# Kernel tuning notes

Measured on AMD Instinct MI355X. Metric: run time of the kernel, lower is better.

The kernel has to match this reference:

```python
import jax, jax.numpy as jnp
import numpy as np

N = 50000
E = 800000
IN_CH = 128
HID = 32
HEADS = 8
OUT_CH = 64
NEG_SLOPE = 0.2


def _gat_layer(x, W, att_src, att_dst, bias, src, dst, H, C, concat):
    """One GATConv layer (add aggregation, self-loops appended).
    x: [n, Fin], W: [Fin, H*C], att_*: [H, C], bias: [H*C] or [C].
    src/dst: [E] int edge endpoints (no self loops; they are appended here).
    """
    n = x.shape[0]
    xs = (x @ W).reshape(n, H, C)                 # projected features [n,H,C]
    a_src = (xs * att_src).sum(-1)                # [n,H]
    a_dst = (xs * att_dst).sum(-1)                # [n,H]
    loop = jnp.arange(n, dtype=src.dtype)
    s = jnp.concatenate([src, loop])              # [E+n]
    d = jnp.concatenate([dst, loop])
    alpha = a_src[s] + a_dst[d]                   # per-edge score [E+n,H]
    alpha = jax.nn.leaky_relu(alpha, NEG_SLOPE)
    # segment softmax over destination node (every node has a self loop,
    # so no empty segments)
    amax = jax.ops.segment_max(alpha, d, num_segments=n)
    ex = jnp.exp(alpha - amax[d])
    denom = jax.ops.segment_sum(ex, d, num_segments=n)
    alpha = ex / denom[d]                         # normalized attention [E+n,H]
    # weighted scatter-add aggregation
    out = jax.ops.segment_sum(alpha[:, :, None] * xs[s], d, num_segments=n)
    out = out.reshape(n, H * C) if concat else out.mean(axis=1)
    return out + bias


def setup_inputs() -> dict:
    key = jax.random.key(0)
    ks = jax.random.split(key, 12)
    def glorot(k, shape):
        fan = shape[0] + shape[-1]
        return jax.random.uniform(k, shape, jnp.float32,
                                  -jnp.sqrt(6.0 / fan), jnp.sqrt(6.0 / fan))
    x = jax.random.normal(ks[0], (N, IN_CH), jnp.float32)
    edge_index = jax.random.randint(ks[1], (2, E), 0, N, dtype=jnp.int64)
    W1 = glorot(ks[2], (IN_CH, HEADS * HID))
    att_src1 = glorot(ks[3], (HEADS, HID))
    att_dst1 = glorot(ks[4], (HEADS, HID))
    bias1 = jnp.zeros((HEADS * HID,), jnp.float32)
    W2 = glorot(ks[5], (HEADS * HID, 1 * OUT_CH))
    att_src2 = glorot(ks[6], (1, OUT_CH))
    att_dst2 = glorot(ks[7], (1, OUT_CH))
    bias2 = jnp.zeros((OUT_CH,), jnp.float32)
    return {"x": x, "edge_index": edge_index,
            "W1": W1, "att_src1": att_src1, "att_dst1": att_dst1, "bias1": bias1,
            "W2": W2, "att_src2": att_src2, "att_dst2": att_dst2, "bias2": bias2}


def reference(x, edge_index, W1, att_src1, att_dst1, bias1,
              W2, att_src2, att_dst2, bias2):
    src, dst = edge_index[0], edge_index[1]
    h = _gat_layer(x, W1, att_src1, att_dst1, bias1, src, dst,
                   HEADS, HID, concat=True)      # [N, HEADS*HID]
    h = jax.nn.elu(h)
    out = _gat_layer(h, W2, att_src2, att_dst2, bias2, src, dst,
                     1, OUT_CH, concat=False)    # [N, OUT_CH]
    return out
```

## Files before the change

### kernel.cpp

```cpp
#include <hip/hip_runtime.h>

#define NN 50000
#define NE 800000
#define IN_CH 128
#define HID 32
#define HEADS 8
#define HC 256
#define OUT_CH 64
#define NEG_SLOPE 0.2f
#define SCAN_BLOCKS 196

typedef _Float16 half4 __attribute__((ext_vector_type(4)));
typedef _Float16 half8 __attribute__((ext_vector_type(8)));
typedef float    f32x4 __attribute__((ext_vector_type(4)));


__global__ void hist_kernel(const int* __restrict__ dst, int* __restrict__ deg) {
    int e = blockIdx.x * blockDim.x + threadIdx.x;
    if (e < NE) atomicAdd(&deg[dst[e]], 1);
}

__global__ __launch_bounds__(256)
void scan_phase1(const int* __restrict__ deg, int* __restrict__ excl,
                 int* __restrict__ bsum) {
    __shared__ int sm[256];
    const int t = blockIdx.x * 256 + threadIdx.x;
    const int v = (t < NN) ? deg[t] : 0;
    sm[threadIdx.x] = v;
    __syncthreads();
    for (int off = 1; off < 256; off <<= 1) {
        int u = (threadIdx.x >= off) ? sm[threadIdx.x - off] : 0;
        __syncthreads();
        sm[threadIdx.x] += u;
        __syncthreads();
    }
    if (t < NN) excl[t] = sm[threadIdx.x] - v;
    if (threadIdx.x == 255) bsum[blockIdx.x] = sm[255];
}

__global__ __launch_bounds__(256)
void scan_phase2(const int* __restrict__ bsum, int* __restrict__ boff,
                 int* __restrict__ offsets) {
    __shared__ int sm[256];
    const int t = threadIdx.x;
    const int v = (t < SCAN_BLOCKS) ? bsum[t] : 0;
    sm[t] = v;
    __syncthreads();
    for (int off = 1; off < 256; off <<= 1) {
        int u = (t >= off) ? sm[t - off] : 0;
        __syncthreads();
        sm[t] += u;
        __syncthreads();
    }
    if (t < SCAN_BLOCKS) boff[t] = sm[t] - v;
    if (t == 255) offsets[NN] = sm[255];
}

__global__ __launch_bounds__(256)
void scan_phase3(const int* __restrict__ excl, const int* __restrict__ boff,
                 int* __restrict__ offsets, int* __restrict__ cursor) {
    const int t = blockIdx.x * 256 + threadIdx.x;
    if (t < NN) {
        int v = excl[t] + boff[blockIdx.x];
        offsets[t] = v;
        cursor[t]  = v;
    }
}

__global__ void scatter_kernel(const int* __restrict__ src,
                               const int* __restrict__ dst,
                               int* __restrict__ cursor, int* __restrict__ ssrc) {
    int e = blockIdx.x * blockDim.x + threadIdx.x;
    if (e < NE) {
        int d = dst[e];
        int pos = atomicAdd(&cursor[d], 1);
        ssrc[pos] = src[e];
    }
}


__global__ void cast_f32_f16(const float* __restrict__ in, _Float16* __restrict__ out,
                             int n8) {
    int i = blockIdx.x * blockDim.x + threadIdx.x;
    if (i >= n8) return;
    float4 a = ((const float4*)in)[i * 2];
    float4 b = ((const float4*)in)[i * 2 + 1];
    half8 h;
    h[0] = (_Float16)a.x; h[1] = (_Float16)a.y; h[2] = (_Float16)a.z; h[3] = (_Float16)a.w;
    h[4] = (_Float16)b.x; h[5] = (_Float16)b.y; h[6] = (_Float16)b.z; h[7] = (_Float16)b.w;
    ((half8*)out)[i] = h;
}

__global__ void transpose_cast(const float* __restrict__ W, _Float16* __restrict__ Wt,
                               int K, int N) {
    int i = blockIdx.x * blockDim.x + threadIdx.x;
    if (i >= K * N) return;
    int k = i / N, n = i - k * N;
    Wt[(size_t)n * K + k] = (_Float16)W[i];
}

__global__ __launch_bounds__(256)
void gemm_mfma_h(const _Float16* __restrict__ A, const _Float16* __restrict__ Bt,
                 _Float16* __restrict__ C, int M, int N, int K) {
    __shared__ _Float16 Asl[64][136];
    __shared__ _Float16 Btl[64][136];
    const int tid  = threadIdx.x;
    const int wave = tid >> 6, lane = tid & 63;
    const int lr = lane & 15, lk = lane >> 4;
    const int bm = blockIdx.x * 64, bn = blockIdx.y * 64;
    const int sr = tid >> 2;
    const int ss = (tid & 3) * 32;

    f32x4 acc[4];
#pragma unroll
    for (int i = 0; i < 4; ++i) acc[i] = (f32x4){0.f, 0.f, 0.f, 0.f};

    for (int k0 = 0; k0 < K; k0 += 128) {
        {
            const int ar = bm + sr;
            half8 v0 = {}, v1 = {}, v2 = {}, v3 = {};
            if (ar < M) {
                const half8* ga = (const half8*)(A + (size_t)ar * K + k0 + ss);
                v0 = ga[0]; v1 = ga[1]; v2 = ga[2]; v3 = ga[3];
            }
            *(half8*)&Asl[sr][ss + 0]  = v0;
            *(half8*)&Asl[sr][ss + 8]  = v1;
            *(half8*)&Asl[sr][ss + 16] = v2;
            *(half8*)&Asl[sr][ss + 24] = v3;
            const half8* gb = (const half8*)(Bt + (size_t)(bn + sr) * K + k0 + ss);
            half8 w0 = gb[0], w1 = gb[1], w2 = gb[2], w3 = gb[3];
            *(half8*)&Btl[sr][ss + 0]  = w0;
            *(half8*)&Btl[sr][ss + 8]  = w1;
            *(half8*)&Btl[sr][ss + 16] = w2;
            *(half8*)&Btl[sr][ss + 24] = w3;
        }
        __syncthreads();
#pragma unroll
        for (int kk = 0; kk < 128; kk += 32) {
            half8 a = *(const half8*)&Asl[wave * 16 + lr][kk + lk * 8];
#pragma unroll
            for (int nt = 0; nt < 4; ++nt) {
                half8 b = *(const half8*)&Btl[nt * 16 + lr][kk + lk * 8];
                acc[nt] = __builtin_amdgcn_mfma_f32_16x16x32_f16(a, b, acc[nt], 0, 0, 0);
            }
        }
        __syncthreads();
    }
#pragma unroll
    for (int nt = 0; nt < 4; ++nt) {
        const int col = bn + nt * 16 + lr;
#pragma unroll
        for (int r = 0; r < 4; ++r) {
            const int m = bm + wave * 16 + lk * 4 + r;
            if (m < M) C[(size_t)m * N + col] = (_Float16)acc[nt][r];
        }
    }
}

__global__ __launch_bounds__(256)
void gemm_mfma_hm(const _Float16* __restrict__ A, const _Float16* __restrict__ Bt,
                  _Float16* __restrict__ C, int M, int N, int K) {
    __shared__ _Float16 Asl[64][136];
    __shared__ _Float16 Btl[64][136];
    const int tid  = threadIdx.x;
    const int wave = tid >> 6, lane = tid & 63;
    const int lr = lane & 15, lk = lane >> 4;
    const int bm = blockIdx.x * 64, bn = blockIdx.y * 64;
    const int sr = tid >> 2;
    const int ss = (tid & 3) * 32;

    f32x4 acc[4];
#pragma unroll
    for (int i = 0; i < 4; ++i) acc[i] = (f32x4){0.f, 0.f, 0.f, 0.f};

    for (int k0 = 0; k0 < K; k0 += 128) {
        {
            const int ar = bm + sr;
            half8 v0 = {}, v1 = {}, v2 = {}, v3 = {};
            if (ar < M) {
                const half8* ga = (const half8*)(A + (size_t)ar * K + k0 + ss);
                v0 = ga[0]; v1 = ga[1]; v2 = ga[2]; v3 = ga[3];
            }
            *(half8*)&Asl[sr][ss + 0]  = v0;
            *(half8*)&Asl[sr][ss + 8]  = v1;
            *(half8*)&Asl[sr][ss + 16] = v2;
            *(half8*)&Asl[sr][ss + 24] = v3;
            const half8* gb = (const half8*)(Bt + (size_t)(bn + sr) * K + k0 + ss);
            half8 w0 = gb[0], w1 = gb[1], w2 = gb[2], w3 = gb[3];
            *(half8*)&Btl[sr][ss + 0]  = w0;
            *(half8*)&Btl[sr][ss + 8]  = w1;
            *(half8*)&Btl[sr][ss + 16] = w2;
            *(half8*)&Btl[sr][ss + 24] = w3;
        }
        __syncthreads();
#pragma unroll
        for (int kk = 0; kk < 128; kk += 32) {
            half8 a = *(const half8*)&Asl[wave * 16 + lr][kk + lk * 8];
#pragma unroll
            for (int nt = 0; nt < 4; ++nt) {
                half8 b = *(const half8*)&Btl[nt * 16 + lr][kk + lk * 8];
                acc[nt] = __builtin_amdgcn_mfma_f32_16x16x32_f16(a, b, acc[nt], 0, 0, 0);
            }
        }
        __syncthreads();
    }
#pragma unroll
    for (int nt = 0; nt < 4; ++nt) {
        const int col = bn + nt * 16 + lr;
        const int hh = col >> 5, cc = col & 31;
#pragma unroll
        for (int r = 0; r < 4; ++r) {
            const int m = bm + wave * 16 + lk * 4 + r;
            if (m < M) C[((size_t)hh * M + m) * 32 + cc] = (_Float16)acc[nt][r];
        }
    }
}


__global__ void attcoef1(const _Float16* __restrict__ xsh, const float* __restrict__ att_s,
                         const float* __restrict__ att_d,
                         float* __restrict__ a_sh, float* __restrict__ a_dh) {
    int n = blockIdx.x * blockDim.x + threadIdx.x;
    int h = blockIdx.y;
    if (n >= NN) return;
    const _Float16* xp = xsh + ((size_t)h * NN + n) * 32;
    const float* sp = att_s + h * 32;
    const float* dp = att_d + h * 32;
    float as = 0.f, ad = 0.f;
#pragma unroll
    for (int i = 0; i < 4; ++i) {
        half8 v = *(const half8*)(xp + i * 8);
#pragma unroll
        for (int j = 0; j < 8; ++j) {
            float f = (float)v[j];
            as += f * sp[i * 8 + j];
            ad += f * dp[i * 8 + j];
        }
    }
    a_sh[(size_t)h * NN + n] = as;
    a_dh[(size_t)h * NN + n] = ad;
}

__global__ void attcoef2(const _Float16* __restrict__ xs, const float* __restrict__ att_s,
                         const float* __restrict__ att_d,
                         float* __restrict__ a_s, float* __restrict__ a_d) {
    int n = blockIdx.x * blockDim.x + threadIdx.x;
    if (n >= NN) return;
    const _Float16* xp = xs + (long)n * 64;
    float as = 0.f, ad = 0.f;
#pragma unroll
    for (int i = 0; i < 8; ++i) {
        half8 v = *(const half8*)(xp + i * 8);
#pragma unroll
        for (int j = 0; j < 8; ++j) {
            float f = (float)v[j];
            as += f * att_s[i * 8 + j];
            ad += f * att_d[i * 8 + j];
        }
    }
    a_s[n] = as;
    a_d[n] = ad;
}


__device__ __forceinline__ float lrelu(float x) { return x > 0.f ? x : NEG_SLOPE * x; }

__global__ __launch_bounds__(256)
void agg1(const _Float16* __restrict__ xsh,
          const float* __restrict__ a_sh,
          const float* __restrict__ a_dh,
          const int* __restrict__ offsets, const int* __restrict__ ssrc,
          const float* __restrict__ bias,
          _Float16* __restrict__ out) {
    const int head = blockIdx.x & 7;
    const int grp  = blockIdx.x >> 3;
    const int wave = threadIdx.x >> 6;
    const int lane = threadIdx.x & 63;
    const int slot = lane >> 3;
    const int j4   = (lane & 7) * 4;
    const int n    = grp * 32 + wave * 8 + slot;
    const bool valid = (n < NN);
    const _Float16* xh = xsh + (size_t)head * NN * 32;
    const float* ash = a_sh + (size_t)head * NN;

    int beg = 0, end = 0;
    float adn = 0.f;
    if (valid) {
        beg = offsets[n];
        end = offsets[n + 1];
        adn = a_dh[(size_t)head * NN + n];
    }
    float den = 0.f, c0 = 0.f, c1 = 0.f, c2 = 0.f, c3 = 0.f;
    int e = beg;
    while (__ballot(e < end) != 0ull) {
        const bool a0 = e < end, a1 = (e + 1) < end;
        const int i0 = a0 ? e : 0, i1 = a1 ? (e + 1) : 0;
        const int s0 = ssrc[i0], s1 = ssrc[i1];
        const float sc0 = ash[s0], sc1 = ash[s1];
        half4 v0 = *(const half4*)(xh + (size_t)s0 * 32 + j4);
        half4 v1 = *(const half4*)(xh + (size_t)s1 * 32 + j4);
        const float p0 = a0 ? __expf(lrelu(sc0 + adn)) : 0.f;
        const float p1 = a1 ? __expf(lrelu(sc1 + adn)) : 0.f;
        den += p0 + p1;
        c0 += p0 * (float)v0[0] + p1 * (float)v1[0];
        c1 += p0 * (float)v0[1] + p1 * (float)v1[1];
        c2 += p0 * (float)v0[2] + p1 * (float)v1[2];
        c3 += p0 * (float)v0[3] + p1 * (float)v1[3];
        e += 2;
    }
    if (valid) {
        const float ps = __expf(lrelu(ash[n] + adn));
        half4 sv = *(const half4*)(xh + (size_t)n * 32 + j4);
        den += ps;
        c0 += ps * (float)sv[0]; c1 += ps * (float)sv[1];
        c2 += ps * (float)sv[2]; c3 += ps * (float)sv[3];
        const float inv = 1.0f / den;
        float4 bb = *(const float4*)(bias + head * 32 + j4);
        float o0 = c0 * inv + bb.x, o1 = c1 * inv + bb.y;
        float o2 = c2 * inv + bb.z, o3 = c3 * inv + bb.w;
        o0 = o0 > 0.f ? o0 : expm1f(o0);
        o1 = o1 > 0.f ? o1 : expm1f(o1);
        o2 = o2 > 0.f ? o2 : expm1f(o2);
        o3 = o3 > 0.f ? o3 : expm1f(o3);
        half4 ho;
        ho[0] = (_Float16)o0; ho[1] = (_Float16)o1;
        ho[2] = (_Float16)o2; ho[3] = (_Float16)o3;
        *(half4*)(out + (size_t)n * HC + head * 32 + j4) = ho;
    }
}

__global__ __launch_bounds__(256)
void agg2(const _Float16* __restrict__ xs,
          const float* __restrict__ a_s, const float* __restrict__ a_d,
          const int* __restrict__ offsets, const int* __restrict__ ssrc,
          const float* __restrict__ bias,
          float* __restrict__ out) {
    const int grp  = blockIdx.x;
    const int wave = threadIdx.x >> 6;
    const int lane = threadIdx.x & 63;
    const int slot = lane >> 3;
    const int j8   = (lane & 7) * 8;
    const int n    = grp * 32 + wave * 8 + slot;
    const bool valid = (n < NN);

    int beg = 0, end = 0;
    float adn = 0.f;
    if (valid) {
        beg = offsets[n];
        end = offsets[n + 1];
        adn = a_d[n];
    }
    float den = 0.f;
    float c[8] = {};
    int e = beg;
    while (__ballot(e < end) != 0ull) {
        const bool a0 = e < end, a1 = (e + 1) < end;
        const int i0 = a0 ? e : 0, i1 = a1 ? (e + 1) : 0;
        const int s0 = ssrc[i0], s1 = ssrc[i1];
        const float sc0 = a_s[s0], sc1 = a_s[s1];
        half8 v0 = *(const half8*)(xs + (size_t)s0 * OUT_CH + j8);
        half8 v1 = *(const half8*)(xs + (size_t)s1 * OUT_CH + j8);
        const float p0 = a0 ? __expf(lrelu(sc0 + adn)) : 0.f;
        const float p1 = a1 ? __expf(lrelu(sc1 + adn)) : 0.f;
        den += p0 + p1;
#pragma unroll
        for (int q = 0; q < 8; ++q)
            c[q] += p0 * (float)v0[q] + p1 * (float)v1[q];
        e += 2;
    }
    if (valid) {
        const float ps = __expf(lrelu(a_s[n] + adn));
        half8 sv = *(const half8*)(xs + (size_t)n * OUT_CH + j8);
        den += ps;
#pragma unroll
        for (int q = 0; q < 8; ++q) c[q] += ps * (float)sv[q];
        const float inv = 1.0f / den;
        float4 w0, w1;
        w0.x = c[0] * inv + bias[j8 + 0];
        w0.y = c[1] * inv + bias[j8 + 1];
        w0.z = c[2] * inv + bias[j8 + 2];
        w0.w = c[3] * inv + bias[j8 + 3];
        w1.x = c[4] * inv + bias[j8 + 4];
        w1.y = c[5] * inv + bias[j8 + 5];
        w1.z = c[6] * inv + bias[j8 + 6];
        w1.w = c[7] * inv + bias[j8 + 7];
        *(float4*)(out + (size_t)n * OUT_CH + j8)     = w0;
        *(float4*)(out + (size_t)n * OUT_CH + j8 + 4) = w1;
    }
}


extern "C" void kernel_launch(void* const* d_in, const int* in_sizes, int n_in,
                              void* d_out, int out_size, void* d_ws, size_t ws_size,
                              hipStream_t stream) {
    const float* x     = (const float*)d_in[0];
    const int*   ei    = (const int*)d_in[1];
    const float* W1    = (const float*)d_in[2];
    const float* atts1 = (const float*)d_in[3];
    const float* attd1 = (const float*)d_in[4];
    const float* bias1 = (const float*)d_in[5];
    const float* W2    = (const float*)d_in[6];
    const float* atts2 = (const float*)d_in[7];
    const float* attd2 = (const float*)d_in[8];
    const float* bias2 = (const float*)d_in[9];
    float*       out   = (float*)d_out;

    const int* srcp = ei;
    const int* dstp = ei + NE;

    char* ws = (char*)d_ws;
    size_t off = 0;
    auto alloc = [&](size_t bytes) -> void* {
        void* p = ws + off;
        off += (bytes + 255) & ~(size_t)255;
        return p;
    };
    _Float16* xh    = (_Float16*)alloc((size_t)NN * IN_CH * 2);
    _Float16* xsh1  = (_Float16*)alloc((size_t)NN * HC * 2);
    _Float16* h1h   = (_Float16*)alloc((size_t)NN * HC * 2);
    _Float16* W1t   = (_Float16*)alloc((size_t)HC * IN_CH * 2);
    _Float16* W2t   = (_Float16*)alloc((size_t)OUT_CH * HC * 2);
    float*    as1   = (float*)alloc((size_t)NN * HEADS * 4);
    float*    ad1   = (float*)alloc((size_t)NN * HEADS * 4);
    int*   deg      = (int*)alloc((size_t)NN * 4);
    int*   offsets  = (int*)alloc((size_t)(NN + 1) * 4);
    int*   cursor   = (int*)alloc((size_t)NN * 4);
    int*   ssrc     = (int*)alloc((size_t)NE * 4);
    int*   excl     = (int*)alloc((size_t)NN * 4);
    int*   bsum     = (int*)alloc((size_t)SCAN_BLOCKS * 4);
    int*   boff     = (int*)alloc((size_t)SCAN_BLOCKS * 4);
    _Float16* xs2h = xsh1;
    float*    as2  = as1;
    float*    ad2  = ad1;

    hipMemsetAsync(deg, 0, (size_t)NN * 4, stream);
    hist_kernel<<<(NE + 255) / 256, 256, 0, stream>>>(dstp, deg);
    scan_phase1<<<SCAN_BLOCKS, 256, 0, stream>>>(deg, excl, bsum);
    scan_phase2<<<1, 256, 0, stream>>>(bsum, boff, offsets);
    scan_phase3<<<SCAN_BLOCKS, 256, 0, stream>>>(excl, boff, offsets, cursor);
    scatter_kernel<<<(NE + 255) / 256, 256, 0, stream>>>(srcp, dstp, cursor, ssrc);

    cast_f32_f16<<<(NN * IN_CH / 8 + 255) / 256, 256, 0, stream>>>(x, xh, NN * IN_CH / 8);
    transpose_cast<<<(IN_CH * HC + 255) / 256, 256, 0, stream>>>(W1, W1t, IN_CH, HC);
    transpose_cast<<<(HC * OUT_CH + 255) / 256, 256, 0, stream>>>(W2, W2t, HC, OUT_CH);

    {
        dim3 grid((NN + 63) / 64, HC / 64);
        gemm_mfma_hm<<<grid, 256, 0, stream>>>(xh, W1t, xsh1, NN, HC, IN_CH);
    }
    {
        dim3 grid((NN + 255) / 256, HEADS);
        attcoef1<<<grid, 256, 0, stream>>>(xsh1, atts1, attd1, as1, ad1);
    }
    agg1<<<((NN + 31) / 32) * 8, 256, 0, stream>>>(xsh1, as1, ad1, offsets, ssrc, bias1, h1h);

    {
        dim3 grid((NN + 63) / 64, OUT_CH / 64);
        gemm_mfma_h<<<grid, 256, 0, stream>>>(h1h, W2t, xs2h, NN, OUT_CH, HC);
    }
    attcoef2<<<(NN + 255) / 256, 256, 0, stream>>>(xs2h, atts2, attd2, as2, ad2);
    agg2<<<(NN + 31) / 32, 256, 0, stream>>>(xs2h, as2, ad2, offsets, ssrc, bias2, out);
}
```

Measured before the change: 326.0 us.

## Precompute per-edge attention weights in separate edge-parallel kernels before aggregation

Adds a sorted destination array and new edge-parallel kernels that compute exp(leaky_relu(a_src+a_dst)) per edge and head once. These are stored in a dense array, and self-loop weights are computed in the coefficient kernels. The aggregation kernels then read contiguous precomputed weights instead of gathering a_src and evaluating exp per edge, and agg1 unrolls to four edges per iteration. In exchange it writes and reads an extra 8×E float buffer plus sdst, adding memory traffic and two kernel launches.

```diff
diff --git a/kernel.cpp b/kernel.cpp
--- a/kernel.cpp
+++ b/kernel.cpp
@@ -69,12 +69,14 @@
 
 __global__ void scatter_kernel(const int* __restrict__ src,
                                const int* __restrict__ dst,
-                               int* __restrict__ cursor, int* __restrict__ ssrc) {
+                               int* __restrict__ cursor, int* __restrict__ ssrc,
+                               int* __restrict__ sdst) {
     int e = blockIdx.x * blockDim.x + threadIdx.x;
     if (e < NE) {
         int d = dst[e];
         int pos = atomicAdd(&cursor[d], 1);
         ssrc[pos] = src[e];
+        sdst[pos] = d;
     }
 }
 
@@ -217,9 +219,13 @@
 }
 
 
+__device__ __forceinline__ float lrelu(float x) { return x > 0.f ? x : NEG_SLOPE * x; }
+
 __global__ void attcoef1(const _Float16* __restrict__ xsh, const float* __restrict__ att_s,
                          const float* __restrict__ att_d,
-                         float* __restrict__ a_sh, float* __restrict__ a_dh) {
+                         float* __restrict__ asn,
+                         float* __restrict__ adn2,
+                         float* __restrict__ pself1) {
     int n = blockIdx.x * blockDim.x + threadIdx.x;
     int h = blockIdx.y;
     if (n >= NN) return;
@@ -237,13 +243,35 @@
             ad += f * dp[i * 8 + j];
         }
     }
-    a_sh[(size_t)h * NN + n] = as;
-    a_dh[(size_t)h * NN + n] = ad;
+    asn[(size_t)n * 8 + h]  = as;
+    adn2[(size_t)n * 8 + h] = ad;
+    pself1[(size_t)h * NN + n] = __expf(lrelu(as + ad));
+}
+
+__global__ void pedge1(const int* __restrict__ ssrc, const int* __restrict__ sdst,
+                       const float* __restrict__ asn, const float* __restrict__ adn2,
+                       float* __restrict__ p1) {
+    int i = blockIdx.x * blockDim.x + threadIdx.x;
+    if (i >= NE) return;
+    int s = ssrc[i], d = sdst[i];
+    float4 A0 = *(const float4*)(asn + (size_t)s * 8);
+    float4 A1 = *(const float4*)(asn + (size_t)s * 8 + 4);
+    float4 D0 = *(const float4*)(adn2 + (size_t)d * 8);
+    float4 D1 = *(const float4*)(adn2 + (size_t)d * 8 + 4);
+    p1[0 * NE + i] = __expf(lrelu(A0.x + D0.x));
+    p1[1 * NE + i] = __expf(lrelu(A0.y + D0.y));
+    p1[2 * NE + i] = __expf(lrelu(A0.z + D0.z));
+    p1[3 * NE + i] = __expf(lrelu(A0.w + D0.w));
+    p1[4 * NE + i] = __expf(lrelu(A1.x + D1.x));
+    p1[5 * NE + i] = __expf(lrelu(A1.y + D1.y));
+    p1[6 * NE + i] = __expf(lrelu(A1.z + D1.z));
+    p1[7 * NE + i] = __expf(lrelu(A1.w + D1.w));
 }
 
 __global__ void attcoef2(const _Float16* __restrict__ xs, const float* __restrict__ att_s,
                          const float* __restrict__ att_d,
-                         float* __restrict__ a_s, float* __restrict__ a_d) {
+                         float* __restrict__ a_s, float* __restrict__ a_d,
+                         float* __restrict__ pself2) {
     int n = blockIdx.x * blockDim.x + threadIdx.x;
     if (n >= NN) return;
     const _Float16* xp = xs + (long)n * 64;
@@ -260,15 +288,22 @@
     }
     a_s[n] = as;
     a_d[n] = ad;
-}
-
-
-__device__ __forceinline__ float lrelu(float x) { return x > 0.f ? x : NEG_SLOPE * x; }
+    pself2[n] = __expf(lrelu(as + ad));
+}
+
+__global__ void pedge2(const int* __restrict__ ssrc, const int* __restrict__ sdst,
+                       const float* __restrict__ a_s, const float* __restrict__ a_d,
+                       float* __restrict__ p2) {
+    int i = blockIdx.x * blockDim.x + threadIdx.x;
+    if (i >= NE) return;
+    p2[i] = __expf(lrelu(a_s[ssrc[i]] + a_d[sdst[i]]));
+}
+
 
 __global__ __launch_bounds__(256)
 void agg1(const _Float16* __restrict__ xsh,
-          const float* __restrict__ a_sh,
-          const float* __restrict__ a_dh,
+          const float* __restrict__ p1,
+          const float* __restrict__ pself1,
           const int* __restrict__ offsets, const int* __restrict__ ssrc,
           const float* __restrict__ bias,
           _Float16* __restrict__ out) {
@@ -281,35 +316,31 @@
     const int n    = grp * 32 + wave * 8 + slot;
     const bool valid = (n < NN);
     const _Float16* xh = xsh + (size_t)head * NN * 32;
-    const float* ash = a_sh + (size_t)head * NN;
+    const float* pe = p1 + (size_t)head * NE;
 
     int beg = 0, end = 0;
-    float adn = 0.f;
-    if (valid) {
-        beg = offsets[n];
-        end = offsets[n + 1];
-        adn = a_dh[(size_t)head * NN + n];
-    }
+    if (valid) { beg = offsets[n]; end = offsets[n + 1]; }
     float den = 0.f, c0 = 0.f, c1 = 0.f, c2 = 0.f, c3 = 0.f;
     int e = beg;
     while (__ballot(e < end) != 0ull) {
-        const bool a0 = e < end, a1 = (e + 1) < end;
-        const int i0 = a0 ? e : 0, i1 = a1 ? (e + 1) : 0;
-        const int s0 = ssrc[i0], s1 = ssrc[i1];
-        const float sc0 = ash[s0], sc1 = ash[s1];
+        const bool a0 = e < end, a1 = e + 1 < end, a2 = e + 2 < end, a3 = e + 3 < end;
+        const int s0 = ssrc[a0 ? e : 0],     s1 = ssrc[a1 ? e + 1 : 0];
+        const int s2 = ssrc[a2 ? e + 2 : 0], s3 = ssrc[a3 ? e + 3 : 0];
+        const float q0 = a0 ? pe[e] : 0.f,     q1 = a1 ? pe[e + 1] : 0.f;
+        const float q2 = a2 ? pe[e + 2] : 0.f, q3 = a3 ? pe[e + 3] : 0.f;
         half4 v0 = *(const half4*)(xh + (size_t)s0 * 32 + j4);
         half4 v1 = *(const half4*)(xh + (size_t)s1 * 32 + j4);
-        const float p0 = a0 ? __expf(lrelu(sc0 + adn)) : 0.f;
-        const float p1 = a1 ? __expf(lrelu(sc1 + adn)) : 0.f;
-        den += p0 + p1;
-        c0 += p0 * (float)v0[0] + p1 * (float)v1[0];
-        c1 += p0 * (float)v0[1] + p1 * (float)v1[1];
-        c2 += p0 * (float)v0[2] + p1 * (float)v1[2];
-        c3 += p0 * (float)v0[3] + p1 * (float)v1[3];
-        e += 2;
+        half4 v2 = *(const half4*)(xh + (size_t)s2 * 32 + j4);
+        half4 v3 = *(const half4*)(xh + (size_t)s3 * 32 + j4);
+        den += (q0 + q1) + (q2 + q3);
+        c0 += q0 * (float)v0[0] + q1 * (float)v1[0] + q2 * (float)v2[0] + q3 * (float)v3[0];
+        c1 += q0 * (float)v0[1] + q1 * (float)v1[1] + q2 * (float)v2[1] + q3 * (float)v3[1];
+        c2 += q0 * (float)v0[2] + q1 * (float)v1[2] + q2 * (float)v2[2] + q3 * (float)v3[2];
+        c3 += q0 * (float)v0[3] + q1 * (float)v1[3] + q2 * (float)v2[3] + q3 * (float)v3[3];
+        e += 4;
     }
     if (valid) {
-        const float ps = __expf(lrelu(ash[n] + adn));
+        const float ps = pself1[(size_t)head * NN + n];
         half4 sv = *(const half4*)(xh + (size_t)n * 32 + j4);
         den += ps;
         c0 += ps * (float)sv[0]; c1 += ps * (float)sv[1];
@@ -331,7 +362,8 @@
 
 __global__ __launch_bounds__(256)
 void agg2(const _Float16* __restrict__ xs,
-          const float* __restrict__ a_s, const float* __restrict__ a_d,
+          const float* __restrict__ p2,
+          const float* __restrict__ pself2,
           const int* __restrict__ offsets, const int* __restrict__ ssrc,
           const float* __restrict__ bias,
           float* __restrict__ out) {
@@ -344,32 +376,24 @@
     const bool valid = (n < NN);
 
     int beg = 0, end = 0;
-    float adn = 0.f;
-    if (valid) {
-        beg = offsets[n];
-        end = offsets[n + 1];
-        adn = a_d[n];
-    }
+    if (valid) { beg = offsets[n]; end = offsets[n + 1]; }
     float den = 0.f;
     float c[8] = {};
     int e = beg;
     while (__ballot(e < end) != 0ull) {
-        const bool a0 = e < end, a1 = (e + 1) < end;
-        const int i0 = a0 ? e : 0, i1 = a1 ? (e + 1) : 0;
-        const int s0 = ssrc[i0], s1 = ssrc[i1];
-        const float sc0 = a_s[s0], sc1 = a_s[s1];
+        const bool a0 = e < end, a1 = e + 1 < end;
+        const int s0 = ssrc[a0 ? e : 0], s1 = ssrc[a1 ? e + 1 : 0];
+        const float q0 = a0 ? p2[e] : 0.f, q1 = a1 ? p2[e + 1] : 0.f;
         half8 v0 = *(const half8*)(xs + (size_t)s0 * OUT_CH + j8);
         half8 v1 = *(const half8*)(xs + (size_t)s1 * OUT_CH + j8);
-        const float p0 = a0 ? __expf(lrelu(sc0 + adn)) : 0.f;
-        const float p1 = a1 ? __expf(lrelu(sc1 + adn)) : 0.f;
-        den += p0 + p1;
+        den += q0 + q1;
 #pragma unroll
         for (int q = 0; q < 8; ++q)
-            c[q] += p0 * (float)v0[q] + p1 * (float)v1[q];
+            c[q] += q0 * (float)v0[q] + q1 * (float)v1[q];
         e += 2;
     }
     if (valid) {
-        const float ps = __expf(lrelu(a_s[n] + adn));
+        const float ps = pself2[n];
         half8 sv = *(const half8*)(xs + (size_t)n * OUT_CH + j8);
         den += ps;
 #pragma unroll
@@ -415,30 +439,35 @@
         off += (bytes + 255) & ~(size_t)255;
         return p;
     };
-    _Float16* xh    = (_Float16*)alloc((size_t)NN * IN_CH * 2);
-    _Float16* xsh1  = (_Float16*)alloc((size_t)NN * HC * 2);
-    _Float16* h1h   = (_Float16*)alloc((size_t)NN * HC * 2);
-    _Float16* W1t   = (_Float16*)alloc((size_t)HC * IN_CH * 2);
-    _Float16* W2t   = (_Float16*)alloc((size_t)OUT_CH * HC * 2);
-    float*    as1   = (float*)alloc((size_t)NN * HEADS * 4);
-    float*    ad1   = (float*)alloc((size_t)NN * HEADS * 4);
+    _Float16* xh     = (_Float16*)alloc((size_t)NN * IN_CH * 2);
+    _Float16* xsh1   = (_Float16*)alloc((size_t)NN * HC * 2);
+    _Float16* h1h    = (_Float16*)alloc((size_t)NN * HC * 2);
+    float*    p1     = (float*)alloc((size_t)HEADS * NE * 4);
+    _Float16* W1t    = (_Float16*)alloc((size_t)HC * IN_CH * 2);
+    _Float16* W2t    = (_Float16*)alloc((size_t)OUT_CH * HC * 2);
+    float*    asn    = (float*)alloc((size_t)NN * 8 * 4);
+    float*    adn2   = (float*)alloc((size_t)NN * 8 * 4);
+    float*    pself1 = (float*)alloc((size_t)HEADS * NN * 4);
+    float*    as2    = (float*)alloc((size_t)NN * 4);
+    float*    ad2    = (float*)alloc((size_t)NN * 4);
+    float*    pself2 = (float*)alloc((size_t)NN * 4);
+    float*    p2     = (float*)alloc((size_t)NE * 4);
     int*   deg      = (int*)alloc((size_t)NN * 4);
     int*   offsets  = (int*)alloc((size_t)(NN + 1) * 4);
     int*   cursor   = (int*)alloc((size_t)NN * 4);
     int*   ssrc     = (int*)alloc((size_t)NE * 4);
+    int*   sdst     = (int*)alloc((size_t)NE * 4);
     int*   excl     = (int*)alloc((size_t)NN * 4);
     int*   bsum     = (int*)alloc((size_t)SCAN_BLOCKS * 4);
     int*   boff     = (int*)alloc((size_t)SCAN_BLOCKS * 4);
     _Float16* xs2h = xsh1;
-    float*    as2  = as1;
-    float*    ad2  = ad1;
 
     hipMemsetAsync(deg, 0, (size_t)NN * 4, stream);
     hist_kernel<<<(NE + 255) / 256, 256, 0, stream>>>(dstp, deg);
     scan_phase1<<<SCAN_BLOCKS, 256, 0, stream>>>(deg, excl, bsum);
     scan_phase2<<<1, 256, 0, stream>>>(bsum, boff, offsets);
     scan_phase3<<<SCAN_BLOCKS, 256, 0, stream>>>(excl, boff, offsets, cursor);
-    scatter_kernel<<<(NE + 255) / 256, 256, 0, stream>>>(srcp, dstp, cursor, ssrc);
+    scatter_kernel<<<(NE + 255) / 256, 256, 0, stream>>>(srcp, dstp, cursor, ssrc, sdst);
 
     cast_f32_f16<<<(NN * IN_CH / 8 + 255) / 256, 256, 0, stream>>>(x, xh, NN * IN_CH / 8);
     transpose_cast<<<(IN_CH * HC + 255) / 256, 256, 0, stream>>>(W1, W1t, IN_CH, HC);
@@ -450,14 +479,16 @@
     }
     {
         dim3 grid((NN + 255) / 256, HEADS);
-        attcoef1<<<grid, 256, 0, stream>>>(xsh1, atts1, attd1, as1, ad1);
-    }
-    agg1<<<((NN + 31) / 32) * 8, 256, 0, stream>>>(xsh1, as1, ad1, offsets, ssrc, bias1, h1h);
+        attcoef1<<<grid, 256, 0, stream>>>(xsh1, atts1, attd1, asn, adn2, pself1);
+    }
+    pedge1<<<(NE + 255) / 256, 256, 0, stream>>>(ssrc, sdst, asn, adn2, p1);
+    agg1<<<((NN + 31) / 32) * 8, 256, 0, stream>>>(xsh1, p1, pself1, offsets, ssrc, bias1, h1h);
 
     {
         dim3 grid((NN + 63) / 64, OUT_CH / 64);
         gemm_mfma_h<<<grid, 256, 0, stream>>>(h1h, W2t, xs2h, NN, OUT_CH, HC);
     }
-    attcoef2<<<(NN + 255) / 256, 256, 0, stream>>>(xs2h, atts2, attd2, as2, ad2);
-    agg2<<<(NN + 31) / 32, 256, 0, stream>>>(xs2h, as2, ad2, offsets, ssrc, bias2, out);
-}
+    attcoef2<<<(NN + 255) / 256, 256, 0, stream>>>(xs2h, atts2, attd2, as2, ad2, pself2);
+    pedge2<<<(NE + 255) / 256, 256, 0, stream>>>(ssrc, sdst, as2, ad2, p2);
+    agg2<<<(NN + 31) / 32, 256, 0, stream>>>(xs2h, p2, pself2, offsets, ssrc, bias2, out);
+}
```

Measured after the change: 325.8 us. No clear change (-0.0%).
